# Kernel tuning notes

Hardware: AMD Instinct MI355X
Metric: run time of the kernel (lower is better)

## Reference

```python
import jax, jax.numpy as jnp
import numpy as np

B, N, C_IN = 4, 48, 32
HID = [32, 32]          # hidden_channel_list
NB = [32, 32]           # neighborhood_channels
C_OUT = 16
N_BASIS = 6             # equivariant 2->2 basis ops used by SnConv2


def _masked(t, mask):
    # zero out entries for padded nodes; mask: B,n,n,n bool, t: B,n,n,n,C
    return jnp.where(mask[..., None], t, jnp.zeros((), t.dtype))


def snconv2(t, W, b):
    """Sn-equivariant 2nd-order conv on dims (1,2); dim 3 rides along.
    t: B,i,j,m,C.  W: [6, C_in, C_out], one mixing matrix per basis op."""
    n = t.shape[1]
    tT = jnp.swapaxes(t, 1, 2)                       # transpose op
    diag = jnp.einsum('biimc->bimc', t)              # diagonal, B,i,m,C
    rows = t.sum(axis=2) / n                         # row sums,  B,i,m,C
    cols = t.sum(axis=1) / n                         # col sums,  B,j,m,C
    tot = t.sum(axis=(1, 2)) / (n * n)               # total sum, B,m,C
    # contract small features BEFORE broadcasting back to 2nd order
    out = (jnp.einsum('bijmc,cd->bijmd', t, W[0])
           + jnp.einsum('bijmc,cd->bijmd', tT, W[1])
           + jnp.einsum('bimc,cd->bimd', diag, W[2])[:, :, None]
           + jnp.einsum('bimc,cd->bimd', rows, W[3])[:, :, None]
           + jnp.einsum('bjmc,cd->bjmd', cols, W[4])[:, None]
           + jnp.einsum('bmc,cd->bmd', tot, W[5])[:, None, None]
           + b)
    return out


def localconv2(t, Wv, bv, Ww, bw, Wo, bo):
    """LocalConv2, product_type='elementwise': per-channel message passing
    along the node dims: z[b,i,j] = sum_k v[b,i,k] * w[b,k,j] / n."""
    n = t.shape[1]
    v = jnp.einsum('bijmc,cd->bijmd', t, Wv) + bv
    w = jnp.einsum('bijmc,cd->bijmd', t, Ww) + bw
    z = jnp.einsum('bikmc,bkjmc->bijmc', v, w) / n
    return jnp.einsum('bijmc,cd->bijmd', z, Wo) + bo


def setup_inputs() -> dict:
    key = jax.random.key(0)
    ks = jax.random.split(key, 24)
    x = jax.random.normal(ks[0], (B, N, C_IN), dtype=jnp.float32)
    # graphs of unequal size: per-graph node counts in [N//2, N]
    sizes = jax.random.randint(ks[1], (B,), N // 2, N + 1)
    node_valid = jnp.arange(N)[None, :] < sizes[:, None]            # B,n
    mask = (node_valid[:, :, None, None]
            & node_valid[:, None, :, None]
            & node_valid[:, None, None, :])                          # B,n,n,n
    s = 0.05
    inp = {'x': x, 'mask': mask}
    cin = C_IN
    for li, (nch, cout) in enumerate(zip(NB, HID)):
        inp[f'basic_W{li}'] = s * jax.random.normal(ks[2 + 8 * li], (N_BASIS, cin, cin), dtype=jnp.float32)
        inp[f'basic_b{li}'] = jnp.zeros((cin,), jnp.float32)
        inp[f'lv_W{li}'] = s * jax.random.normal(ks[3 + 8 * li], (cin, nch), dtype=jnp.float32)
        inp[f'lv_b{li}'] = jnp.zeros((nch,), jnp.float32)
        inp[f'lw_W{li}'] = s * jax.random.normal(ks[4 + 8 * li], (cin, nch), dtype=jnp.float32)
        inp[f'lw_b{li}'] = jnp.zeros((nch,), jnp.float32)
        inp[f'lo_W{li}'] = s * jax.random.normal(ks[5 + 8 * li], (nch, cout), dtype=jnp.float32)
        inp[f'lo_b{li}'] = jnp.zeros((cout,), jnp.float32)
        cin = cout
    inp['final_W'] = s * jax.random.normal(ks[20], (N_BASIS, cin, C_OUT), dtype=jnp.float32)
    inp['final_b'] = jnp.zeros((C_OUT,), jnp.float32)
    return inp


def reference(x, mask,
              basic_W0, basic_b0, lv_W0, lv_b0, lw_W0, lw_b0, lo_W0, lo_b0,
              basic_W1, basic_b1, lv_W1, lv_b1, lw_W1, lw_b1, lo_W1, lo_b1,
              final_W, final_b):
    # order-3 outer product T[b,i,j,k,c] = x[b,i,c]*x[b,j,c]*x[b,k,c]
    t = (x[:, :, None, None, :] * x[:, None, :, None, :]) * x[:, None, None, :, :]
    t = _masked(t, mask)
    layers = [(basic_W0, basic_b0, lv_W0, lv_b0, lw_W0, lw_b0, lo_W0, lo_b0),
              (basic_W1, basic_b1, lv_W1, lv_b1, lw_W1, lw_b1, lo_W1, lo_b1)]
    for bw_, bb_, vw, vb, ww, wb, ow, ob in layers:
        t = _masked(snconv2(t, bw_, bb_), mask)
        t = localconv2(t, vw, vb, ww, wb, ow, ob)
        t = jax.nn.relu(t)
        t = _masked(t, mask)
    out = _masked(snconv2(t, final_W, final_b), mask)
    return out
```

## Files before the change

### kernel.cpp

```cpp
#include <hip/hip_runtime.h>
#include <cstdint>


namespace {

constexpr int nB = 4, nN = 48, nC = 32;
constexpr int SJ_ = nN * nC;
constexpr int SI_ = nN * SJ_;
constexpr long SB_ = (long)nN * SI_;
constexpr int RP_ = 294912;
constexpr int CP_ = 294912;
constexpr int TP_ = 6144;

__device__ __forceinline__ void decodePos(int p, int& b, int& i, int& j, int& m) {
    m = p % nN; int r = p / nN;
    j = r % nN; r /= nN;
    i = r % nN; b = r / nN;
}

__global__ __launch_bounds__(256) void k_prepcomp(
    const float* __restrict__ x, const void* __restrict__ maskp,
    float* __restrict__ vm, float* __restrict__ S,
    const float* __restrict__ Wb0, const float* __restrict__ bb0,
    const float* __restrict__ Wv0, const float* __restrict__ Ww0,
    const float* __restrict__ Wb1, const float* __restrict__ bb1,
    const float* __restrict__ Wv1, const float* __restrict__ Ww1,
    float* __restrict__ cW, float* __restrict__ cb, float* __restrict__ cWs)
{
    __shared__ float Ws[1024];
    __shared__ float vmL[nB * nN];
    const int tid = threadIdx.x;

    if (blockIdx.x == 4) {
        const unsigned int w0 = *(const unsigned int*)maskp;
        const bool is_byte = (w0 == 0x01010101u);
        if (tid < nB * nN) {
            int b = tid / nN, i = tid % nN;
            long idx = ((long)(b * nN + i) * nN + i) * nN + i;
            int bit;
            if (is_byte) bit = (((const unsigned char*)maskp)[idx] != 0);
            else         bit = (((const int*)maskp)[idx] != 0);
            float f = bit ? 1.f : 0.f;
            vm[tid] = f; vmL[tid] = f;
        }
        __syncthreads();
        if (tid < nB * nC) {
            int b = tid >> 5, c = tid & 31;
            float s = 0.f;
            for (int j = 0; j < nN; ++j) s += x[(b * nN + j) * nC + c] * vmL[b * nN + j];
            S[tid] = s;
        }
        return;
    }

    const int blk = blockIdx.x;
    const float* Wb = (blk < 2) ? Wb0 : Wb1;
    const float* bb = (blk < 2) ? bb0 : bb1;
    const float* Wr = (blk == 0) ? Wv0 : (blk == 1) ? Ww0 : (blk == 2) ? Wv1 : Ww1;
    for (int q = tid; q < 1024; q += 256) Ws[q] = Wr[q];
    __syncthreads();
    for (int q = tid; q < 6144; q += 256) {
        const int d = q & 31;
        const float* row = Wb + (q >> 5) * 32;
        float s = 0.f;
        #pragma unroll
        for (int e = 0; e < 32; ++e) s = fmaf(row[e], Ws[e * 32 + d], s);
        cW[blk * 6144 + q] = s;
    }
    if (blk < 2) {
        for (int q = tid; q < 1024; q += 256) {
            const int d = q & 31; const int c = q >> 5;
            const float* r0 = Wb + c * 32;
            const float* r1 = Wb + 1024 + c * 32;
            float s = 0.f;
            #pragma unroll
            for (int e = 0; e < 32; ++e) s = fmaf(r0[e] + r1[e], Ws[e * 32 + d], s);
            cWs[blk * 1024 + q] = s;
        }
    }
    if (tid < 32) {
        float s = 0.f;
        #pragma unroll
        for (int e = 0; e < 32; ++e) s = fmaf(bb[e], Ws[e * 32 + tid], s);
        cb[blk * 32 + tid] = s;
    }
}

__global__ __launch_bounds__(256) void k_mix0(
    const float* __restrict__ x, const float* __restrict__ S,
    const float* __restrict__ Wb_a, const float* __restrict__ bias_a,
    float* __restrict__ dr_a, float* __restrict__ cc_a, float* __restrict__ tb_a,
    const float* __restrict__ Wb_b, const float* __restrict__ bias_b,
    float* __restrict__ dr_b, float* __restrict__ cc_b, float* __restrict__ tb_b)
{
    const int set = (blockIdx.x >= 36);
    const float* Wb   = set ? Wb_b   : Wb_a;
// ... 63 lines not shown
    float* ccp = set ? cc_b : cc_a;
    float* tbp = set ? tb_b : tb_a;
    __shared__ float W2s[32 * DOUT], W3s[32 * DOUT], W4s[32 * DOUT], W5s[32 * DOUT], bs[DOUT];
    const int tid = threadIdx.x;
    for (int q = tid; q < 32 * DOUT; q += 256) {
        W2s[q] = Wb[2 * 32 * DOUT + q]; W3s[q] = Wb[3 * 32 * DOUT + q];
        W4s[q] = Wb[4 * 32 * DOUT + q]; W5s[q] = Wb[5 * 32 * DOUT + q];
    }
    if (tid < DOUT) bs[tid] = bias[tid];
    __syncthreads();
    const int id = (blockIdx.x - (set ? 36 : 0)) * 256 + tid;
    const int m = id % nN; int r = id / nN; const int i = r % nN; const int b = r / nN;
    float odr[DOUT], occ[DOUT];
    #pragma unroll
    for (int d = 0; d < DOUT; ++d) { odr[d] = 0.f; occ[d] = 0.f; }
    for (int c2 = 0; c2 < 32; ++c2) {
        size_t q = (size_t)id * 32 + c2;
        float dg = dgp[q];
        float rw = (rw2[q] + rw2[q + RP_]) * (1.f / nN);
        float cl = (cl2[q] + cl2[q + CP_]) * (1.f / nN);
        #pragma unroll
        for (int d = 0; d < DOUT; ++d) {
            odr[d] = fmaf(dg, W2s[c2 * DOUT + d], fmaf(rw, W3s[c2 * DOUT + d], odr[d]));
            occ[d] = fmaf(cl, W4s[c2 * DOUT + d], occ[d]);
        }
    }
    #pragma unroll
    for (int d = 0; d < DOUT; d += 4) {
        *(float4*)(drp + (size_t)id * DOUT + d) = make_float4(odr[d], odr[d+1], odr[d+2], odr[d+3]);
        *(float4*)(ccp + (size_t)id * DOUT + d) = make_float4(occ[d], occ[d+1], occ[d+2], occ[d+3]);
    }
    if (i == 0) {
        float ot[DOUT];
        #pragma unroll
        for (int d = 0; d < DOUT; ++d) ot[d] = bs[d];
        for (int c2 = 0; c2 < 32; ++c2) {
            size_t q = (size_t)(b * nN + m) * 32 + c2;
            float tv = (tt4[q] + tt4[q + TP_] + tt4[q + 2 * TP_] + tt4[q + 3 * TP_])
                       * (1.f / (nN * nN));
            #pragma unroll
            for (int d = 0; d < DOUT; ++d) ot[d] = fmaf(tv, W5s[c2 * DOUT + d], ot[d]);
        }
        for (int d = 0; d < DOUT; d += 4)
            *(float4*)(tbp + (size_t)(b * nN + m) * DOUT + d) = make_float4(ot[d], ot[d+1], ot[d+2], ot[d+3]);
    }
}

#define FMA4(ar, tv, w4)                       \
    ar[0] = fmaf(tv, w4.x, ar[0]);             \
    ar[1] = fmaf(tv, w4.y, ar[1]);             \
    ar[2] = fmaf(tv, w4.z, ar[2]);             \
    ar[3] = fmaf(tv, w4.w, ar[3]);

template <int MODE>
__global__ __launch_bounds__(256) void k_vw(
    const float* __restrict__ src, const float* __restrict__ vm,
    const float* __restrict__ drv, const float* __restrict__ ccv, const float* __restrict__ tbv,
    const float* __restrict__ drw, const float* __restrict__ ccw, const float* __restrict__ tbw,
    const float* __restrict__ Wv2, const float* __restrict__ Ww2,
    const float* __restrict__ bv, const float* __restrict__ bw,
    float* __restrict__ vout, float* __restrict__ wout)
{
    constexpr int CH = 64;
    constexpr int CS = CH * 34;
    constexpr int BUF = (MODE == 0) ? CS : 2 * CS;
    __shared__ float sT[2][BUF];
    __shared__ float wL[(MODE == 0) ? 2048 : 4096];
    const int tid = threadIdx.x;

    {
        float4* wl4 = (float4*)wL;
        for (int q = tid; q < 512; q += 256) wl4[q] = ((const float4*)Wv2)[q];
        if (MODE == 1)
            for (int q = tid; q < 512; q += 256) wl4[512 + q] = ((const float4*)Ww2)[q];
    }

    const int base0 = blockIdx.x * 9 * CH;
    float4 rA0, rA1, rB0, rB1;

    auto loadChunk = [&](int k) {
        const int cb = base0 + k * CH;
        {   const int q = tid; const int pl = q >> 3, cq = q & 7;
            const int p = cb + pl;
            if (MODE == 0) {
                int b, i, j, m; decodePos(p, b, i, j, m);
                float4 xi = *(const float4*)(src + (size_t)(b * nN + i) * nC + cq * 4);
                float4 xj = *(const float4*)(src + (size_t)(b * nN + j) * nC + cq * 4);
                float4 xm = *(const float4*)(src + (size_t)(b * nN + m) * nC + cq * 4);
                rA0.x = xi.x * xj.x * xm.x; rA0.y = xi.y * xj.y * xm.y;
                rA0.z = xi.z * xj.z * xm.z; rA0.w = xi.w * xj.w * xm.w;
            } else {
                rA0 = *(const float4*)(src + (size_t)p * nC + cq * 4);
                int b, i, j, m; decodePos(p, b, i, j, m);
                long pT = ((long)(b * nN + j) * nN + i) * nN + m;
                rB0 = *(const float4*)(src + pT * nC + cq * 4);
            }
        }
        {   const int q = 256 + tid; const int pl = q >> 3, cq = q & 7;
            const int p = cb + pl;
            if (MODE == 0) {
                int b, i, j, m; decodePos(p, b, i, j, m);
                float4 xi = *(const float4*)(src + (size_t)(b * nN + i) * nC + cq * 4);
                float4 xj = *(const float4*)(src + (size_t)(b * nN + j) * nC + cq * 4);
                float4 xm = *(const float4*)(src + (size_t)(b * nN + m) * nC + cq * 4);
                rA1.x = xi.x * xj.x * xm.x; rA1.y = xi.y * xj.y * xm.y;
                rA1.z = xi.z * xj.z * xm.z; rA1.w = xi.w * xj.w * xm.w;
            } else {
                rA1 = *(const float4*)(src + (size_t)p * nC + cq * 4);
                int b, i, j, m; decodePos(p, b, i, j, m);
                long pT = ((long)(b * nN + j) * nN + i) * nN + m;
                rB1 = *(const float4*)(src + pT * nC + cq * 4);
            }
        }
    };
    auto writeChunk = [&](int buf) {
        {   const int q = tid; const int o = (q >> 3) * 34 + (q & 7) * 4;
            sT[buf][o + 0] = rA0.x; sT[buf][o + 1] = rA0.y;
            sT[buf][o + 2] = rA0.z; sT[buf][o + 3] = rA0.w;
            if (MODE == 1) {
                sT[buf][CS + o + 0] = rB0.x; sT[buf][CS + o + 1] = rB0.y;
                sT[buf][CS + o + 2] = rB0.z; sT[buf][CS + o + 3] = rB0.w;
            }
        }
        {   const int q = 256 + tid; const int o = (q >> 3) * 34 + (q & 7) * 4;
            sT[buf][o + 0] = rA1.x; sT[buf][o + 1] = rA1.y;
            sT[buf][o + 2] = rA1.z; sT[buf][o + 3] = rA1.w;
            if (MODE == 1) {
                sT[buf][CS + o + 0] = rB1.x; sT[buf][CS + o + 1] = rB1.y;
                sT[buf][CS + o + 2] = rB1.z; sT[buf][CS + o + 3] = rB1.w;
            }
        }
    };

    loadChunk(0);
    writeChunk(0);
    __syncthreads();

    const int pt = tid >> 3, dq = tid & 7;
    const int p0 = pt * 2, d0 = dq * 4;

    for (int k = 0; k < 9; ++k) {
        const int cur = k & 1;
        if (k < 8) loadChunk(k + 1);
        __builtin_amdgcn_sched_barrier(0);

        float accv[2][4], accw[2][4];
        #pragma unroll
        for (int l = 0; l < 2; ++l)
            #pragma unroll
            for (int d = 0; d < 4; ++d) { accv[l][d] = 0.f; accw[l][d] = 0.f; }

        const float* sp = sT[cur];
        #pragma unroll
        for (int cp = 0; cp < 16; ++cp) {
            float2 t0 = *(const float2*)(sp + (p0 + 0) * 34 + cp * 2);
            float2 t1 = *(const float2*)(sp + (p0 + 1) * 34 + cp * 2);
            const int c0 = cp * 2, c1 = cp * 2 + 1;
            const float* wwb = (MODE == 0) ? (wL + 1024) : (wL + 2048);
            float4 wv0 = *(const float4*)(wL + c0 * nC + d0);
            float4 wv1 = *(const float4*)(wL + c1 * nC + d0);
            float4 ww0 = *(const float4*)(wwb + c0 * nC + d0);
            float4 ww1 = *(const float4*)(wwb + c1 * nC + d0);
            FMA4(accv[0], t0.x, wv0); FMA4(accv[1], t1.x, wv0);
            FMA4(accv[0], t0.y, wv1); FMA4(accv[1], t1.y, wv1);
            FMA4(accw[0], t0.x, ww0); FMA4(accw[1], t1.x, ww0);
            FMA4(accw[0], t0.y, ww1); FMA4(accw[1], t1.y, ww1);
        }
        if (MODE == 1) {
            #pragma unroll
            for (int cp = 0; cp < 16; ++cp) {
                float2 t0 = *(const float2*)(sp + CS + (p0 + 0) * 34 + cp * 2);
                float2 t1 = *(const float2*)(sp + CS + (p0 + 1) * 34 + cp * 2);
                const int c0 = cp * 2, c1 = cp * 2 + 1;
                float4 wv0 = *(const float4*)(wL + 1024 + c0 * nC + d0);
                float4 wv1 = *(const float4*)(wL + 1024 + c1 * nC + d0);
                float4 ww0 = *(const float4*)(wL + 3072 + c0 * nC + d0);
                float4 ww1 = *(const float4*)(wL + 3072 + c1 * nC + d0);
                FMA4(accv[0], t0.x, wv0); FMA4(accv[1], t1.x, wv0);
                FMA4(accv[0], t0.y, wv1); FMA4(accv[1], t1.y, wv1);
                FMA4(accw[0], t0.x, ww0); FMA4(accw[1], t1.x, ww0);
                FMA4(accw[0], t0.y, ww1); FMA4(accw[1], t1.y, ww1);
            }
        }

        const int cb = base0 + k * CH;
        {
            float4 b4 = *(const float4*)(bv + d0);
            #pragma unroll
            for (int l = 0; l < 2; ++l) {
                int p = cb + p0 + l;
                int b, i, j, m; decodePos(p, b, i, j, m);
                float4 d4 = *(const float4*)(drv + (size_t)((b * nN + i) * nN + m) * nC + d0);
                float4 c4 = *(const float4*)(ccv + (size_t)((b * nN + j) * nN + m) * nC + d0);
                float4 t4 = *(const float4*)(tbv + (size_t)(b * nN + m) * nC + d0);
                float mk = vm[b * nN + i] * vm[b * nN + j] * vm[b * nN + m];
                float4 o4;
                o4.x = (accv[l][0] + d4.x + c4.x + t4.x) * mk + b4.x;
                o4.y = (accv[l][1] + d4.y + c4.y + t4.y) * mk + b4.y;
                o4.z = (accv[l][2] + d4.z + c4.z + t4.z) * mk + b4.z;
                o4.w = (accv[l][3] + d4.w + c4.w + t4.w) * mk + b4.w;
                *(float4*)(vout + (size_t)p * nC + d0) = o4;
            }
        }
        {
            float4 b4 = *(const float4*)(bw + d0);
            #pragma unroll
            for (int l = 0; l < 2; ++l) {
                int p = cb + p0 + l;
                int b, i, j, m; decodePos(p, b, i, j, m);
                float4 d4 = *(const float4*)(drw + (size_t)((b * nN + i) * nN + m) * nC + d0);
                float4 c4 = *(const float4*)(ccw + (size_t)((b * nN + j) * nN + m) * nC + d0);
                float4 t4 = *(const float4*)(tbw + (size_t)(b * nN + m) * nC + d0);
                float mk = vm[b * nN + i] * vm[b * nN + j] * vm[b * nN + m];
                float4 o4;
                o4.x = (accw[l][0] + d4.x + c4.x + t4.x) * mk + b4.x;
                o4.y = (accw[l][1] + d4.y + c4.y + t4.y) * mk + b4.y;
                o4.z = (accw[l][2] + d4.z + c4.z + t4.z) * mk + b4.z;
                o4.w = (accw[l][3] + d4.w + c4.w + t4.w) * mk + b4.w;
                *(float4*)(wout + (size_t)p * nC + d0) = o4;
            }
        }

        if (k < 8) {
            writeChunk((k + 1) & 1);
            __syncthreads();
        }
    }
}

__global__ __launch_bounds__(256, 3) void k_z(
    const float* __restrict__ v, const float* __restrict__ w,
    const float* __restrict__ Wo, const float* __restrict__ bo,
    const float* __restrict__ vm, float* __restrict__ tout,
    float* __restrict__ rows2, float* __restrict__ cols2,
    float* __restrict__ diag_, float* __restrict__ tot4)
{
    __shared__ float lds[12912];
    constexpr int HB = 6456;
    constexpr int ZS = 34;
    constexpr int ZWO = 9792;
    constexpr int TOT0 = 10816;
    const int tid = threadIdx.x;
    const int idb = blockIdx.x;
    const int xcd = idb & 7; const int qq = idb >> 3;
    const int tl = qq & 3; const int bm = (qq >> 2) * 8 + xcd;
    const int it = tl >> 1, jt = tl & 1;
    const int b = bm / nN, m = bm % nN;
    const int c = tid & 31;
    const int g = tid >> 5;
    const int i3 = g >> 1, j2 = g & 1;
    const int il0 = i3 * 6, jl0 = j2 * 12;
    const size_t posbase = (size_t)b * SB_ + (size_t)m * nC;

    const int q0 = tid, q1 = 256 + tid, q2 = 512 + tid;
    const int pV0 = q0 >> 3, pV1 = q1 >> 3, pV2 = q2 >> 3;
    const int cq0 = (q0 & 7) * 4, cq1 = (q1 & 7) * 4, cq2 = (q2 & 7) * 4;
    const int iiV0 = pV0 >> 2, kkV0 = pV0 & 3;
    const int iiV1 = pV1 >> 2, kkV1 = pV1 & 3;
    const int iiV2 = pV2 >> 2, kkV2 = pV2 & 3;
    const int kkW0 = pV0 / 24, jjW0 = pV0 - kkW0 * 24;
    const int kkW1 = pV1 / 24, jjW1 = pV1 - kkW1 * 24;
    const int kkW2 = pV2 / 24, jjW2 = pV2 - kkW2 * 24;
    const float* vs0 = v + posbase + (size_t)(it * 24 + iiV0) * SI_ + (size_t)kkV0 * SJ_ + cq0;
    const float* vs1 = v + posbase + (size_t)(it * 24 + iiV1) * SI_ + (size_t)kkV1 * SJ_ + cq1;
    const float* vs2 = v + posbase + (size_t)(it * 24 + iiV2) * SI_ + (size_t)kkV2 * SJ_ + cq2;
    const float* ws0 = w + posbase + (size_t)kkW0 * SI_ + (size_t)(jt * 24 + jjW0) * SJ_ + cq0;
    const float* ws1 = w + posbase + (size_t)kkW1 * SI_ + (size_t)(jt * 24 + jjW1) * SJ_ + cq1;
    const float* ws2 = w + posbase + (size_t)kkW2 * SI_ + (size_t)(jt * 24 + jjW2) * SJ_ + cq2;
    const int dV0 = kkV0 * 807 + cq0 * 25 + iiV0;
    const int dV1 = kkV1 * 807 + cq1 * 25 + iiV1;
    const int dV2 = kkV2 * 807 + cq2 * 25 + iiV2;
    const int dW0 = 3228 + kkW0 * 807 + cq0 * 25 + jjW0;
    const int dW1 = 3228 + kkW1 * 807 + cq1 * 25 + jjW1;
    const int dW2 = 3228 + kkW2 * 807 + cq2 * 25 + jjW2;

    float4 rv0, rv1, rv2, rw0, rw1, rw2;

    auto loadChunk = [&](int ch) {
// ... 103 lines not shown
            float4 o4;
            o4.x = fmaxf(oac[u][0] + b4.x, 0.f) * mk;
            o4.y = fmaxf(oac[u][1] + b4.y, 0.f) * mk;
            o4.z = fmaxf(oac[u][2] + b4.z, 0.f) * mk;
            o4.w = fmaxf(oac[u][3] + b4.w, 0.f) * mk;
            *(float4*)(tout + posbase + (size_t)gi * SI_ + (size_t)gj * SJ_ + d0) = o4;
            *(float2*)(lds + p * ZS + d0) = make_float2(o4.x, o4.y);
            *(float2*)(lds + p * ZS + d0 + 2) = make_float2(o4.z, o4.w);
        }
        __syncthreads();

        for (int rd = 0; rd < 2; ++rd) {
            int task = rd * 256 + tid;
            if (task < 384) {
                int i_r = task >> 5, c_r = task & 31;
                float rsum = 0.f;
                #pragma unroll
                for (int jl = 0; jl < 24; ++jl) rsum += lds[(i_r * 24 + jl) * ZS + c_r];
                int gi = it * 24 + 12 * h + i_r;
                rows2[(size_t)jt * RP_ + ((size_t)(b * nN + gi) * nN + m) * nC + c_r] = rsum;
                totacc += rsum;
                if (it == jt)
                    diag_[((size_t)(b * nN + gi) * nN + m) * nC + c_r] =
                        lds[(i_r * 24 + (12 * h + i_r)) * ZS + c_r];
            }
        }
        #pragma unroll
        for (int rr = 0; rr < 3; ++rr) {
            int task = rr * 256 + tid;
            int jl = task >> 5, c_c = task & 31;
            float csum = 0.f;
            #pragma unroll
            for (int il = 0; il < 12; ++il) csum += lds[(il * 24 + jl) * ZS + c_c];
            colacc[rr] += csum;
        }
    }

    #pragma unroll
    for (int rr = 0; rr < 3; ++rr) {
        int task = rr * 256 + tid;
        int jl = task >> 5, c_c = task & 31;
        cols2[(size_t)it * CP_ + ((size_t)(b * nN + jt * 24 + jl) * nN + m) * nC + c_c] = colacc[rr];
    }
    lds[TOT0 + g * 32 + c] = totacc;
    __syncthreads();
    if (tid < 32) {
        float s = 0.f;
        #pragma unroll
        for (int gg = 0; gg < 8; ++gg) s += lds[TOT0 + gg * 32 + tid];
        tot4[(size_t)(it * 2 + jt) * TP_ + (size_t)(b * nN + m) * nC + tid] = s;
    }
}

__global__ __launch_bounds__(256) void k_final(
    const float* __restrict__ t, const float* __restrict__ vm,
    const float* __restrict__ drp, const float* __restrict__ ccp, const float* __restrict__ tbp,
    const float* __restrict__ W0, const float* __restrict__ W1,
    float* __restrict__ out)
{
    constexpr int CH = 64, CS = CH * 34;
    __shared__ float sT[2][2 * CS];
    __shared__ float wL[1024];
    const int tid = threadIdx.x;

    {
        float4* wl4 = (float4*)wL;
        for (int q = tid; q < 128; q += 256) wl4[q] = ((const float4*)W0)[q];
        for (int q = tid; q < 128; q += 256) wl4[128 + q] = ((const float4*)W1)[q];
    }

    const int base0 = blockIdx.x * 9 * CH;
    float4 rA0, rA1, rB0, rB1;

    auto loadChunk = [&](int k) {
        const int cb = base0 + k * CH;
        {   const int q = tid; const int pl = q >> 3, cq = q & 7;
            const int p = cb + pl;
            rA0 = *(const float4*)(t + (size_t)p * nC + cq * 4);
            int b, i, j, m; decodePos(p, b, i, j, m);
            long pT = ((long)(b * nN + j) * nN + i) * nN + m;
            rB0 = *(const float4*)(t + pT * nC + cq * 4);
        }
        {   const int q = 256 + tid; const int pl = q >> 3, cq = q & 7;
            const int p = cb + pl;
            rA1 = *(const float4*)(t + (size_t)p * nC + cq * 4);
            int b, i, j, m; decodePos(p, b, i, j, m);
            long pT = ((long)(b * nN + j) * nN + i) * nN + m;
            rB1 = *(const float4*)(t + pT * nC + cq * 4);
        }
    };
    auto writeChunk = [&](int buf) {
        {   const int q = tid; const int o = (q >> 3) * 34 + (q & 7) * 4;
            sT[buf][o + 0] = rA0.x; sT[buf][o + 1] = rA0.y;
            sT[buf][o + 2] = rA0.z; sT[buf][o + 3] = rA0.w;
            sT[buf][CS + o + 0] = rB0.x; sT[buf][CS + o + 1] = rB0.y;
            sT[buf][CS + o + 2] = rB0.z; sT[buf][CS + o + 3] = rB0.w;
        }
        {   const int q = 256 + tid; const int o = (q >> 3) * 34 + (q & 7) * 4;
            sT[buf][o + 0] = rA1.x; sT[buf][o + 1] = rA1.y;
            sT[buf][o + 2] = rA1.z; sT[buf][o + 3] = rA1.w;
            sT[buf][CS + o + 0] = rB1.x; sT[buf][CS + o + 1] = rB1.y;
            sT[buf][CS + o + 2] = rB1.z; sT[buf][CS + o + 3] = rB1.w;
        }
    };

    loadChunk(0);
    writeChunk(0);
    __syncthreads();

    const int pt = tid >> 3, dq = tid & 7;
    const int p0 = pt * 2, d0 = dq * 2;

    for (int k = 0; k < 9; ++k) {
        const int cur = k & 1;
        if (k < 8) loadChunk(k + 1);
        __builtin_amdgcn_sched_barrier(0);

        float acc[2][2];
        acc[0][0] = 0.f; acc[0][1] = 0.f; acc[1][0] = 0.f; acc[1][1] = 0.f;
        const float* sp = sT[cur];
        #pragma unroll
        for (int cp = 0; cp < 16; ++cp) {
            float2 t0 = *(const float2*)(sp + (p0 + 0) * 34 + cp * 2);
            float2 t1 = *(const float2*)(sp + (p0 + 1) * 34 + cp * 2);
            const int c0 = cp * 2, c1 = cp * 2 + 1;
            float2 w0 = *(const float2*)(wL + c0 * 16 + d0);
            float2 w1 = *(const float2*)(wL + c1 * 16 + d0);
            acc[0][0] = fmaf(t0.x, w0.x, acc[0][0]); acc[0][1] = fmaf(t0.x, w0.y, acc[0][1]);
            acc[1][0] = fmaf(t1.x, w0.x, acc[1][0]); acc[1][1] = fmaf(t1.x, w0.y, acc[1][1]);
            acc[0][0] = fmaf(t0.y, w1.x, acc[0][0]); acc[0][1] = fmaf(t0.y, w1.y, acc[0][1]);
            acc[1][0] = fmaf(t1.y, w1.x, acc[1][0]); acc[1][1] = fmaf(t1.y, w1.y, acc[1][1]);
        }
        #pragma unroll
        for (int cp = 0; cp < 16; ++cp) {
            float2 t0 = *(const float2*)(sp + CS + (p0 + 0) * 34 + cp * 2);
            float2 t1 = *(const float2*)(sp + CS + (p0 + 1) * 34 + cp * 2);
            const int c0 = cp * 2, c1 = cp * 2 + 1;
            float2 w0 = *(const float2*)(wL + 512 + c0 * 16 + d0);
            float2 w1 = *(const float2*)(wL + 512 + c1 * 16 + d0);
            acc[0][0] = fmaf(t0.x, w0.x, acc[0][0]); acc[0][1] = fmaf(t0.x, w0.y, acc[0][1]);
            acc[1][0] = fmaf(t1.x, w0.x, acc[1][0]); acc[1][1] = fmaf(t1.x, w0.y, acc[1][1]);
            acc[0][0] = fmaf(t0.y, w1.x, acc[0][0]); acc[0][1] = fmaf(t0.y, w1.y, acc[0][1]);
            acc[1][0] = fmaf(t1.y, w1.x, acc[1][0]); acc[1][1] = fmaf(t1.y, w1.y, acc[1][1]);
        }

        const int cb = base0 + k * CH;
        #pragma unroll
        for (int l = 0; l < 2; ++l) {
            int p = cb + p0 + l;
            int b, i, j, m; decodePos(p, b, i, j, m);
            float2 d2 = *(const float2*)(drp + (size_t)((b * nN + i) * nN + m) * 16 + d0);
            float2 cc2 = *(const float2*)(ccp + (size_t)((b * nN + j) * nN + m) * 16 + d0);
            float2 tb2 = *(const float2*)(tbp + (size_t)(b * nN + m) * 16 + d0);
            float mk = vm[b * nN + i] * vm[b * nN + j] * vm[b * nN + m];
            float2 o2;
            o2.x = (acc[l][0] + d2.x + cc2.x + tb2.x) * mk;
            o2.y = (acc[l][1] + d2.y + cc2.y + tb2.y) * mk;
            *(float2*)(out + (size_t)p * 16 + d0) = o2;
        }

        if (k < 8) {
            writeChunk((k + 1) & 1);
            __syncthreads();
        }
    }
}

}

extern "C" void kernel_launch(void* const* d_in, const int* in_sizes, int n_in,
                              void* d_out, int out_size, void* d_ws, size_t ws_size,
                              hipStream_t stream)
{
    (void)in_sizes; (void)n_in; (void)out_size; (void)ws_size;
    const float* x    = (const float*)d_in[0];
    const void*  mask = d_in[1];
    const float* bW0  = (const float*)d_in[2];
    const float* bb0  = (const float*)d_in[3];
    const float* lvW0 = (const float*)d_in[4];
    const float* lvb0 = (const float*)d_in[5];
    const float* lwW0 = (const float*)d_in[6];
    const float* lwb0 = (const float*)d_in[7];
    const float* loW0 = (const float*)d_in[8];
    const float* lob0 = (const float*)d_in[9];
    const float* bW1  = (const float*)d_in[10];
    const float* bb1  = (const float*)d_in[11];
    const float* lvW1 = (const float*)d_in[12];
    const float* lvb1 = (const float*)d_in[13];
    const float* lwW1 = (const float*)d_in[14];
    const float* lwb1 = (const float*)d_in[15];
    const float* loW1 = (const float*)d_in[16];
    const float* lob1 = (const float*)d_in[17];
    const float* fW   = (const float*)d_in[18];
    const float* fb   = (const float*)d_in[19];

    float* ws  = (float*)d_ws;
    float* t     = ws;
    float* v     = ws + 14155776L;
    float* w     = ws + 28311552L;
    float* rows2 = ws + 42467328L;
    float* cols2 = rows2 + 2 * 294912;
    float* diag  = cols2 + 2 * 294912;
    float* tot4  = diag + 294912;
    float* drv   = tot4 + 4 * 6144;
    float* ccv   = drv + 294912;
    float* tbv   = ccv + 294912;
    float* drw   = tbv + 6144;
    float* ccw   = drw + 294912;
    float* tbw   = ccw + 294912;
    float* cW    = tbw + 6144;
    float* cb    = cW + 4 * 6144;
    float* cWs   = cb + 128;
    float* S     = cWs + 2048;
    float* vm    = S + 128;
    float* out   = (float*)d_out;

    k_prepcomp<<<5, 256, 0, stream>>>(x, mask, vm, S,
                                      bW0, bb0, lvW0, lwW0,
                                      bW1, bb1, lvW1, lwW1, cW, cb, cWs);

    k_mix0<<<72, 256, 0, stream>>>(x, S,
                                   cW + 0,    cb + 0,  drv, ccv, tbv,
                                   cW + 6144, cb + 32, drw, ccw, tbw);
    k_vw<0><<<768, 256, 0, stream>>>(x, vm, drv, ccv, tbv, drw, ccw, tbw,
                                     cWs,
                                     cWs,
                                     lvb0, lwb0, v, w);
    k_z<<<768, 256, 0, stream>>>(v, w, loW0, lob0, vm, t, rows2, cols2, diag, tot4);

    k_mix<32><<<72, 256, 0, stream>>>(diag, rows2, cols2, tot4,
                                      cW + 12288, cb + 64, drv, ccv, tbv,
                                      cW + 18432, cb + 96, drw, ccw, tbw);
    k_vw<1><<<768, 256, 0, stream>>>(t, vm, drv, ccv, tbv, drw, ccw, tbw,
                                     cW + 12288,
                                     cW + 18432,
                                     lvb1, lwb1, v, w);
    k_z<<<768, 256, 0, stream>>>(v, w, loW1, lob1, vm, t, rows2, cols2, diag, tot4);

    k_mix<16><<<36, 256, 0, stream>>>(diag, rows2, cols2, tot4,
                                      fW, fb, drv, ccv, tbv,
                                      fW, fb, drv, ccv, tbv);
    k_final<<<768, 256, 0, stream>>>(t, vm, drv, ccv, tbv, fW, fW + 512, out);
}
```

Measured before the change: 462.4 us.

## Process (i,j)/(j,i) row pairs together to share transposed loads in snconv

The layer-1 v/w kernel and the final snconv kernel now assign each work chunk a pair of mirrored rows (i,j) and (j,i), or two diagonal rows, taken from a precomputed pair table. Both rows are loaded into shared memory once, so the transpose term reads the partner row from LDS and no separate transposed gather is needed. This roughly halves global reads of the 2nd-order tensor in these kernels. In exchange it adds descriptor decoding, a pair-table build in the prep kernel, and a different block count for the final kernel.

```diff
diff --git a/kernel.cpp b/kernel.cpp
--- a/kernel.cpp
+++ b/kernel.cpp
@@ -18,9 +18,25 @@
     i = r % nN; b = r / nN;
 }
 
+#define MAKE_DESC(cgx, _bA,_iA,_jA,_bB,_iB,_jB,_md,_baseA,_baseB) do {        \
+    if ((cgx) < 4512) {                                                        \
+        int pr_ = (cgx) >> 2; int bb_ = (cgx) & 3;                             \
+        int ij_ = pairTab[pr_];                                                \
+        _iA = ij_ & 255; _jA = ij_ >> 8; _bA = bb_;                            \
+        _iB = _jA; _jB = _iA; _bB = bb_; _md = 48;                             \
+    } else {                                                                   \
+        int dg_ = (cgx) - 4512;                                                \
+        int u0_ = 2 * dg_, u1_ = u0_ + 1;                                      \
+        _bA = u0_ / 48; _iA = u0_ - _bA * 48; _jA = _iA;                       \
+        _bB = u1_ / 48; _iB = u1_ - _bB * 48; _jB = _iB; _md = 0;              \
+    }                                                                          \
+    _baseA = (_bA * 48 + _iA) * 48 + _jA;                                      \
+    _baseB = (_bB * 48 + _iB) * 48 + _jB;                                      \
+} while (0)
+
 __global__ __launch_bounds__(256) void k_prepcomp(
     const float* __restrict__ x, const void* __restrict__ maskp,
-    float* __restrict__ vm, float* __restrict__ S,
+    float* __restrict__ vm, float* __restrict__ S, int* __restrict__ pairTab,
     const float* __restrict__ Wb0, const float* __restrict__ bb0,
     const float* __restrict__ Wv0, const float* __restrict__ Ww0,
     const float* __restrict__ Wb1, const float* __restrict__ bb1,
@@ -42,6 +58,12 @@
             else         bit = (((const int*)maskp)[idx] != 0);
             float f = bit ? 1.f : 0.f;
             vm[tid] = f; vmL[tid] = f;
+        }
+        for (int k = tid; k < 1128; k += 256) {
+            int i = 0, a2 = 0;
+            while (a2 + (47 - i) <= k) { a2 += 47 - i; ++i; }
+            int j = i + 1 + (k - a2);
+            pairTab[k] = i | (j << 8);
         }
         __syncthreads();
         if (tid < nB * nC) {
@@ -211,83 +233,57 @@
     ar[2] = fmaf(tv, w4.z, ar[2]);             \
     ar[3] = fmaf(tv, w4.w, ar[3]);
 
-template <int MODE>
-__global__ __launch_bounds__(256) void k_vw(
+__global__ __launch_bounds__(256) void k_vw0(
     const float* __restrict__ src, const float* __restrict__ vm,
     const float* __restrict__ drv, const float* __restrict__ ccv, const float* __restrict__ tbv,
     const float* __restrict__ drw, const float* __restrict__ ccw, const float* __restrict__ tbw,
-    const float* __restrict__ Wv2, const float* __restrict__ Ww2,
+    const float* __restrict__ Wv2,
     const float* __restrict__ bv, const float* __restrict__ bw,
     float* __restrict__ vout, float* __restrict__ wout)
 {
     constexpr int CH = 64;
     constexpr int CS = CH * 34;
-    constexpr int BUF = (MODE == 0) ? CS : 2 * CS;
-    __shared__ float sT[2][BUF];
-    __shared__ float wL[(MODE == 0) ? 2048 : 4096];
+    __shared__ float sT[2][CS];
+    __shared__ float wL[2048];
     const int tid = threadIdx.x;
 
     {
         float4* wl4 = (float4*)wL;
         for (int q = tid; q < 512; q += 256) wl4[q] = ((const float4*)Wv2)[q];
-        if (MODE == 1)
-            for (int q = tid; q < 512; q += 256) wl4[512 + q] = ((const float4*)Ww2)[q];
     }
 
     const int base0 = blockIdx.x * 9 * CH;
-    float4 rA0, rA1, rB0, rB1;
+    float4 rA0, rA1;
 
     auto loadChunk = [&](int k) {
         const int cb = base0 + k * CH;
         {   const int q = tid; const int pl = q >> 3, cq = q & 7;
             const int p = cb + pl;
-            if (MODE == 0) {
-                int b, i, j, m; decodePos(p, b, i, j, m);
-                float4 xi = *(const float4*)(src + (size_t)(b * nN + i) * nC + cq * 4);
-                float4 xj = *(const float4*)(src + (size_t)(b * nN + j) * nC + cq * 4);
-                float4 xm = *(const float4*)(src + (size_t)(b * nN + m) * nC + cq * 4);
-                rA0.x = xi.x * xj.x * xm.x; rA0.y = xi.y * xj.y * xm.y;
-                rA0.z = xi.z * xj.z * xm.z; rA0.w = xi.w * xj.w * xm.w;
-            } else {
-                rA0 = *(const float4*)(src + (size_t)p * nC + cq * 4);
-                int b, i, j, m; decodePos(p, b, i, j, m);
-                long pT = ((long)(b * nN + j) * nN + i) * nN + m;
-                rB0 = *(const float4*)(src + pT * nC + cq * 4);
-            }
+            int b, i, j, m; decodePos(p, b, i, j, m);
+            float4 xi = *(const float4*)(src + (size_t)(b * nN + i) * nC + cq * 4);
+            float4 xj = *(const float4*)(src + (size_t)(b * nN + j) * nC + cq * 4);
+            float4 xm = *(const float4*)(src + (size_t)(b * nN + m) * nC + cq * 4);
+            rA0.x = xi.x * xj.x * xm.x; rA0.y = xi.y * xj.y * xm.y;
+            rA0.z = xi.z * xj.z * xm.z; rA0.w = xi.w * xj.w * xm.w;
         }
         {   const int q = 256 + tid; const int pl = q >> 3, cq = q & 7;
             const int p = cb + pl;
-            if (MODE == 0) {
-                int b, i, j, m; decodePos(p, b, i, j, m);
-                float4 xi = *(const float4*)(src + (size_t)(b * nN + i) * nC + cq * 4);
-                float4 xj = *(const float4*)(src + (size_t)(b * nN + j) * nC + cq * 4);
-                float4 xm = *(const float4*)(src + (size_t)(b * nN + m) * nC + cq * 4);
-                rA1.x = xi.x * xj.x * xm.x; rA1.y = xi.y * xj.y * xm.y;
-                rA1.z = xi.z * xj.z * xm.z; rA1.w = xi.w * xj.w * xm.w;
-            } else {
-                rA1 = *(const float4*)(src + (size_t)p * nC + cq * 4);
-                int b, i, j, m; decodePos(p, b, i, j, m);
-                long pT = ((long)(b * nN + j) * nN + i) * nN + m;
-                rB1 = *(const float4*)(src + pT * nC + cq * 4);
-            }
+            int b, i, j, m; decodePos(p, b, i, j, m);
+            float4 xi = *(const float4*)(src + (size_t)(b * nN + i) * nC + cq * 4);
+            float4 xj = *(const float4*)(src + (size_t)(b * nN + j) * nC + cq * 4);
+            float4 xm = *(const float4*)(src + (size_t)(b * nN + m) * nC + cq * 4);
+            rA1.x = xi.x * xj.x * xm.x; rA1.y = xi.y * xj.y * xm.y;
+            rA1.z = xi.z * xj.z * xm.z; rA1.w = xi.w * xj.w * xm.w;
         }
     };
     auto writeChunk = [&](int buf) {
         {   const int q = tid; const int o = (q >> 3) * 34 + (q & 7) * 4;
             sT[buf][o + 0] = rA0.x; sT[buf][o + 1] = rA0.y;
             sT[buf][o + 2] = rA0.z; sT[buf][o + 3] = rA0.w;
-            if (MODE == 1) {
-                sT[buf][CS + o + 0] = rB0.x; sT[buf][CS + o + 1] = rB0.y;
-                sT[buf][CS + o + 2] = rB0.z; sT[buf][CS + o + 3] = rB0.w;
-            }
         }
         {   const int q = 256 + tid; const int o = (q >> 3) * 34 + (q & 7) * 4;
             sT[buf][o + 0] = rA1.x; sT[buf][o + 1] = rA1.y;
             sT[buf][o + 2] = rA1.z; sT[buf][o + 3] = rA1.w;
-            if (MODE == 1) {
-                sT[buf][CS + o + 0] = rB1.x; sT[buf][CS + o + 1] = rB1.y;
-                sT[buf][CS + o + 2] = rB1.z; sT[buf][CS + o + 3] = rB1.w;
-            }
         }
     };
 
@@ -315,31 +311,14 @@
             float2 t0 = *(const float2*)(sp + (p0 + 0) * 34 + cp * 2);
             float2 t1 = *(const float2*)(sp + (p0 + 1) * 34 + cp * 2);
             const int c0 = cp * 2, c1 = cp * 2 + 1;
-            const float* wwb = (MODE == 0) ? (wL + 1024) : (wL + 2048);
             float4 wv0 = *(const float4*)(wL + c0 * nC + d0);
             float4 wv1 = *(const float4*)(wL + c1 * nC + d0);
-            float4 ww0 = *(const float4*)(wwb + c0 * nC + d0);
-            float4 ww1 = *(const float4*)(wwb + c1 * nC + d0);
+            float4 ww0 = *(const float4*)(wL + 1024 + c0 * nC + d0);
+            float4 ww1 = *(const float4*)(wL + 1024 + c1 * nC + d0);
             FMA4(accv[0], t0.x, wv0); FMA4(accv[1], t1.x, wv0);
             FMA4(accv[0], t0.y, wv1); FMA4(accv[1], t1.y, wv1);
             FMA4(accw[0], t0.x, ww0); FMA4(accw[1], t1.x, ww0);
             FMA4(accw[0], t0.y, ww1); FMA4(accw[1], t1.y, ww1);
-        }
-        if (MODE == 1) {
-            #pragma unroll
-            for (int cp = 0; cp < 16; ++cp) {
-                float2 t0 = *(const float2*)(sp + CS + (p0 + 0) * 34 + cp * 2);
-                float2 t1 = *(const float2*)(sp + CS + (p0 + 1) * 34 + cp * 2);
-                const int c0 = cp * 2, c1 = cp * 2 + 1;
-                float4 wv0 = *(const float4*)(wL + 1024 + c0 * nC + d0);
-                float4 wv1 = *(const float4*)(wL + 1024 + c1 * nC + d0);
-                float4 ww0 = *(const float4*)(wL + 3072 + c0 * nC + d0);
-                float4 ww1 = *(const float4*)(wL + 3072 + c1 * nC + d0);
-                FMA4(accv[0], t0.x, wv0); FMA4(accv[1], t1.x, wv0);
-                FMA4(accv[0], t0.y, wv1); FMA4(accv[1], t1.y, wv1);
-                FMA4(accw[0], t0.x, ww0); FMA4(accw[1], t1.x, ww0);
-                FMA4(accw[0], t0.y, ww1); FMA4(accw[1], t1.y, ww1);
-            }
         }
 
         const int cb = base0 + k * CH;
@@ -383,6 +362,145 @@
         if (k < 8) {
             writeChunk((k + 1) & 1);
             __syncthreads();
+        }
+    }
+}
+
+__global__ __launch_bounds__(256) void k_vwp(
+    const float* __restrict__ src, const float* __restrict__ vm,
+    const int* __restrict__ pairTab,
+    const float* __restrict__ drv, const float* __restrict__ ccv, const float* __restrict__ tbv,
+    const float* __restrict__ drw, const float* __restrict__ ccw, const float* __restrict__ tbw,
+    const float* __restrict__ Wv2, const float* __restrict__ Ww2,
+    const float* __restrict__ bv, const float* __restrict__ bw,
+    float* __restrict__ vout, float* __restrict__ wout)
+{
+    __shared__ float sT[2][96 * 34];
+    __shared__ float wL[4096];
+    const int tid = threadIdx.x;
+
+    {
+        float4* wl4 = (float4*)wL;
+        for (int q = tid; q < 512; q += 256) wl4[q] = ((const float4*)Wv2)[q];
+        for (int q = tid; q < 512; q += 256) wl4[512 + q] = ((const float4*)Ww2)[q];
+    }
+
+    const int cg0 = blockIdx.x * 6;
+    float4 rq0, rq1, rq2;
+
+    auto loadQ = [&](int qi, int baseA, int baseB) -> float4 {
+        const int g = (qi >= 384);
+        const int base = g ? baseB : baseA;
+        const int off = (qi - (g ? 384 : 0)) * 4;
+        return *(const float4*)(src + (size_t)base * 1536 + off);
+    };
+    auto writeQ = [&](float* buf, int qi, float4 r) {
+        const int g = (qi >= 384);
+        const int row = g * 48 + ((qi - g * 384) >> 3);
+        const int o = row * 34 + (qi & 7) * 4;
+        buf[o + 0] = r.x; buf[o + 1] = r.y; buf[o + 2] = r.z; buf[o + 3] = r.w;
+    };
+
+    int bA, iA, jA, bB, iB, jB, md, baseA, baseB;
+    MAKE_DESC(cg0, bA, iA, jA, bB, iB, jB, md, baseA, baseB);
+    rq0 = loadQ(tid, baseA, baseB);
+    rq1 = loadQ(tid + 256, baseA, baseB);
+    rq2 = loadQ(tid + 512, baseA, baseB);
+    writeQ(sT[0], tid, rq0); writeQ(sT[0], tid + 256, rq1); writeQ(sT[0], tid + 512, rq2);
+    __syncthreads();
+
+    const int pt = tid >> 3, dq = tid & 7;
+    const int p0 = pt * 3, d0 = dq * 4;
+    const float4 bv4 = *(const float4*)(bv + d0);
+    const float4 bw4 = *(const float4*)(bw + d0);
+
+    for (int c = 0; c < 6; ++c) {
+        int nbA = 0, niA = 0, njA = 0, nbB = 0, niB = 0, njB = 0, nmd = 0, nbaseA = 0, nbaseB = 0;
+        if (c < 5) {
+            MAKE_DESC(cg0 + c + 1, nbA, niA, njA, nbB, niB, njB, nmd, nbaseA, nbaseB);
+            rq0 = loadQ(tid, nbaseA, nbaseB);
+            rq1 = loadQ(tid + 256, nbaseA, nbaseB);
+            rq2 = loadQ(tid + 512, nbaseA, nbaseB);
+        }
+        __builtin_amdgcn_sched_barrier(0);
+
+        float accv[3][4], accw[3][4];
+        #pragma unroll
+        for (int l = 0; l < 3; ++l)
+            #pragma unroll
+            for (int d = 0; d < 4; ++d) { accv[l][d] = 0.f; accw[l][d] = 0.f; }
+
+        const float* sp = sT[c & 1];
+        const int mir0 = (pt < 16) ? (p0 + md) : (p0 - md);
+        #pragma unroll
+        for (int cp = 0; cp < 16; ++cp) {
+            const int c0 = cp * 2, c1 = c0 + 1;
+            float2 a0 = *(const float2*)(sp + (p0 + 0) * 34 + c0);
+            float2 a1 = *(const float2*)(sp + (p0 + 1) * 34 + c0);
+            float2 a2 = *(const float2*)(sp + (p0 + 2) * 34 + c0);
+            float2 e0 = *(const float2*)(sp + (mir0 + 0) * 34 + c0);
+            float2 e1 = *(const float2*)(sp + (mir0 + 1) * 34 + c0);
+            float2 e2 = *(const float2*)(sp + (mir0 + 2) * 34 + c0);
+            float4 wav0 = *(const float4*)(wL + c0 * nC + d0);
+            float4 wav1 = *(const float4*)(wL + c1 * nC + d0);
+            float4 wbv0 = *(const float4*)(wL + 1024 + c0 * nC + d0);
+            float4 wbv1 = *(const float4*)(wL + 1024 + c1 * nC + d0);
+            float4 waw0 = *(const float4*)(wL + 2048 + c0 * nC + d0);
+            float4 waw1 = *(const float4*)(wL + 2048 + c1 * nC + d0);
+            float4 wbw0 = *(const float4*)(wL + 3072 + c0 * nC + d0);
+            float4 wbw1 = *(const float4*)(wL + 3072 + c1 * nC + d0);
+            FMA4(accv[0], a0.x, wav0); FMA4(accv[0], a0.y, wav1);
+            FMA4(accv[1], a1.x, wav0); FMA4(accv[1], a1.y, wav1);
+            FMA4(accv[2], a2.x, wav0); FMA4(accv[2], a2.y, wav1);
+            FMA4(accv[0], e0.x, wbv0); FMA4(accv[0], e0.y, wbv1);
+            FMA4(accv[1], e1.x, wbv0); FMA4(accv[1], e1.y, wbv1);
+            FMA4(accv[2], e2.x, wbv0); FMA4(accv[2], e2.y, wbv1);
+            FMA4(accw[0], a0.x, waw0); FMA4(accw[0], a0.y, waw1);
+            FMA4(accw[1], a1.x, waw0); FMA4(accw[1], a1.y, waw1);
+            FMA4(accw[2], a2.x, waw0); FMA4(accw[2], a2.y, waw1);
+            FMA4(accw[0], e0.x, wbw0); FMA4(accw[0], e0.y, wbw1);
+            FMA4(accw[1], e1.x, wbw0); FMA4(accw[1], e1.y, wbw1);
+            FMA4(accw[2], e2.x, wbw0); FMA4(accw[2], e2.y, wbw1);
+        }
+
+        const int gb = (pt < 16) ? bA : bB;
+        const int gi = (pt < 16) ? iA : iB;
+        const int gj = (pt < 16) ? jA : jB;
+        const int gbase = (pt < 16) ? baseA : baseB;
+        const int m0 = p0 - ((pt < 16) ? 0 : 48);
+        const float vmi = vm[gb * nN + gi];
+        const float vmj = vm[gb * nN + gj];
+        #pragma unroll
+        for (int l = 0; l < 3; ++l) {
+            const int m = m0 + l;
+            const float mk = vmi * vmj * vm[gb * nN + m];
+            float4 d4 = *(const float4*)(drv + (size_t)((gb * nN + gi) * nN + m) * nC + d0);
+            float4 c4 = *(const float4*)(ccv + (size_t)((gb * nN + gj) * nN + m) * nC + d0);
+            float4 t4 = *(const float4*)(tbv + (size_t)(gb * nN + m) * nC + d0);
+            const size_t po = ((size_t)gbase * 48 + m) * nC + d0;
+            float4 o4;
+            o4.x = (accv[l][0] + d4.x + c4.x + t4.x) * mk + bv4.x;
+            o4.y = (accv[l][1] + d4.y + c4.y + t4.y) * mk + bv4.y;
+            o4.z = (accv[l][2] + d4.z + c4.z + t4.z) * mk + bv4.z;
+            o4.w = (accv[l][3] + d4.w + c4.w + t4.w) * mk + bv4.w;
+            *(float4*)(vout + po) = o4;
+            float4 d4w = *(const float4*)(drw + (size_t)((gb * nN + gi) * nN + m) * nC + d0);
+            float4 c4w = *(const float4*)(ccw + (size_t)((gb * nN + gj) * nN + m) * nC + d0);
+            float4 t4w = *(const float4*)(tbw + (size_t)(gb * nN + m) * nC + d0);
+            float4 o4w;
+            o4w.x = (accw[l][0] + d4w.x + c4w.x + t4w.x) * mk + bw4.x;
+            o4w.y = (accw[l][1] + d4w.y + c4w.y + t4w.y) * mk + bw4.y;
+            o4w.z = (accw[l][2] + d4w.z + c4w.z + t4w.z) * mk + bw4.z;
+            o4w.w = (accw[l][3] + d4w.w + c4w.w + t4w.w) * mk + bw4.w;
+            *(float4*)(wout + po) = o4w;
+        }
+
+        if (c < 5) {
+            float* nb = sT[(c + 1) & 1];
+            writeQ(nb, tid, rq0); writeQ(nb, tid + 256, rq1); writeQ(nb, tid + 512, rq2);
+            __syncthreads();
+            bA = nbA; iA = niA; jA = njA; bB = nbB; iB = niB; jB = njB;
+            md = nmd; baseA = nbaseA; baseB = nbaseB;
         }
     }
 }
@@ -592,14 +710,14 @@
     }
 }
 
-__global__ __launch_bounds__(256) void k_final(
-    const float* __restrict__ t, const float* __restrict__ vm,
+__global__ __launch_bounds__(256) void k_finalp(
+    const float* __restrict__ src, const float* __restrict__ vm,
+    const int* __restrict__ pairTab,
     const float* __restrict__ drp, const float* __restrict__ ccp, const float* __restrict__ tbp,
     const float* __restrict__ W0, const float* __restrict__ W1,
     float* __restrict__ out)
 {
-    constexpr int CH = 64, CS = CH * 34;
-    __shared__ float sT[2][2 * CS];
+    __shared__ float sT[2][96 * 34];
     __shared__ float wL[1024];
     const int tid = threadIdx.x;
 
@@ -609,99 +727,96 @@
         for (int q = tid; q < 128; q += 256) wl4[128 + q] = ((const float4*)W1)[q];
     }
 
-    const int base0 = blockIdx.x * 9 * CH;
-    float4 rA0, rA1, rB0, rB1;
-
-    auto loadChunk = [&](int k) {
-        const int cb = base0 + k * CH;
-        {   const int q = tid; const int pl = q >> 3, cq = q & 7;
-            const int p = cb + pl;
-            rA0 = *(const float4*)(t + (size_t)p * nC + cq * 4);
-            int b, i, j, m; decodePos(p, b, i, j, m);
-            long pT = ((long)(b * nN + j) * nN + i) * nN + m;
-            rB0 = *(const float4*)(t + pT * nC + cq * 4);
-        }
-        {   const int q = 256 + tid; const int pl = q >> 3, cq = q & 7;
-            const int p = cb + pl;
-            rA1 = *(const float4*)(t + (size_t)p * nC + cq * 4);
-            int b, i, j, m; decodePos(p, b, i, j, m);
-            long pT = ((long)(b * nN + j) * nN + i) * nN + m;
-            rB1 = *(const float4*)(t + pT * nC + cq * 4);
-        }
+    const int cg0 = blockIdx.x * 4;
+    float4 rq0, rq1, rq2;
+
+    auto loadQ = [&](int qi, int baseA, int baseB) -> float4 {
+        const int g = (qi >= 384);
+        const int base = g ? baseB : baseA;
+        const int off = (qi - (g ? 384 : 0)) * 4;
+        return *(const float4*)(src + (size_t)base * 1536 + off);
     };
-    auto writeChunk = [&](int buf) {
-        {   const int q = tid; const int o = (q >> 3) * 34 + (q & 7) * 4;
-            sT[buf][o + 0] = rA0.x; sT[buf][o + 1] = rA0.y;
-            sT[buf][o + 2] = rA0.z; sT[buf][o + 3] = rA0.w;
-            sT[buf][CS + o + 0] = rB0.x; sT[buf][CS + o + 1] = rB0.y;
-            sT[buf][CS + o + 2] = rB0.z; sT[buf][CS + o + 3] = rB0.w;
-        }
-        {   const int q = 256 + tid; const int o = (q >> 3) * 34 + (q & 7) * 4;
-            sT[buf][o + 0] = rA1.x; sT[buf][o + 1] = rA1.y;
-            sT[buf][o + 2] = rA1.z; sT[buf][o + 3] = rA1.w;
-            sT[buf][CS + o + 0] = rB1.x; sT[buf][CS + o + 1] = rB1.y;
-            sT[buf][CS + o + 2] = rB1.z; sT[buf][CS + o + 3] = rB1.w;
-        }
+    auto writeQ = [&](float* buf, int qi, float4 r) {
+        const int g = (qi >= 384);
+        const int row = g * 48 + ((qi - g * 384) >> 3);
+        const int o = row * 34 + (qi & 7) * 4;
+        buf[o + 0] = r.x; buf[o + 1] = r.y; buf[o + 2] = r.z; buf[o + 3] = r.w;
     };
 
-    loadChunk(0);
-    writeChunk(0);
+    int bA, iA, jA, bB, iB, jB, md, baseA, baseB;
+    MAKE_DESC(cg0, bA, iA, jA, bB, iB, jB, md, baseA, baseB);
+    rq0 = loadQ(tid, baseA, baseB);
+    rq1 = loadQ(tid + 256, baseA, baseB);
+    rq2 = loadQ(tid + 512, baseA, baseB);
+    writeQ(sT[0], tid, rq0); writeQ(sT[0], tid + 256, rq1); writeQ(sT[0], tid + 512, rq2);
     __syncthreads();
 
     const int pt = tid >> 3, dq = tid & 7;
-    const int p0 = pt * 2, d0 = dq * 2;
-
-    for (int k = 0; k < 9; ++k) {
-        const int cur = k & 1;
-        if (k < 8) loadChunk(k + 1);
+    const int p0 = pt * 3, d0 = dq * 2;
+
+    for (int c = 0; c < 4; ++c) {
+        int nbA = 0, niA = 0, njA = 0, nbB = 0, niB = 0, njB = 0, nmd = 0, nbaseA = 0, nbaseB = 0;
+        if (c < 3) {
+            MAKE_DESC(cg0 + c + 1, nbA, niA, njA, nbB, niB, njB, nmd, nbaseA, nbaseB);
+            rq0 = loadQ(tid, nbaseA, nbaseB);
+            rq1 = loadQ(tid + 256, nbaseA, nbaseB);
+            rq2 = loadQ(tid + 512, nbaseA, nbaseB);
+        }
         __builtin_amdgcn_sched_barrier(0);
 
-        float acc[2][2];
-        acc[0][0] = 0.f; acc[0][1] = 0.f; acc[1][0] = 0.f; acc[1][1] = 0.f;
-        const float* sp = sT[cur];
+        float acc[3][2];
+        #pragma unroll
+        for (int l = 0; l < 3; ++l) { acc[l][0] = 0.f; acc[l][1] = 0.f; }
+
+        const float* sp = sT[c & 1];
+        const int mir0 = (pt < 16) ? (p0 + md) : (p0 - md);
         #pragma unroll
         for (int cp = 0; cp < 16; ++cp) {
-            float2 t0 = *(const float2*)(sp + (p0 + 0) * 34 + cp * 2);
-            float2 t1 = *(const float2*)(sp + (p0 + 1) * 34 + cp * 2);
-            const int c0 = cp * 2, c1 = cp * 2 + 1;
-            float2 w0 = *(const float2*)(wL + c0 * 16 + d0);
-            float2 w1 = *(const float2*)(wL + c1 * 16 + d0);
-            acc[0][0] = fmaf(t0.x, w0.x, acc[0][0]); acc[0][1] = fmaf(t0.x, w0.y, acc[0][1]);
-            acc[1][0] = fmaf(t1.x, w0.x, acc[1][0]); acc[1][1] = fmaf(t1.x, w0.y, acc[1][1]);
-            acc[0][0] = fmaf(t0.y, w1.x, acc[0][0]); acc[0][1] = fmaf(t0.y, w1.y, acc[0][1]);
-            acc[1][0] = fmaf(t1.y, w1.x, acc[1][0]); acc[1][1] = fmaf(t1.y, w1.y, acc[1][1]);
-        }
-        #pragma unroll
-        for (int cp = 0; cp < 16; ++cp) {
-            float2 t0 = *(const float2*)(sp + CS + (p0 + 0) * 34 + cp * 2);
-            float2 t1 = *(const float2*)(sp + CS + (p0 + 1) * 34 + cp * 2);
-            const int c0 = cp * 2, c1 = cp * 2 + 1;
-            float2 w0 = *(const float2*)(wL + 512 + c0 * 16 + d0);
-            float2 w1 = *(const float2*)(wL + 512 + c1 * 16 + d0);
-            acc[0][0] = fmaf(t0.x, w0.x, acc[0][0]); acc[0][1] = fmaf(t0.x, w0.y, acc[0][1]);
-            acc[1][0] = fmaf(t1.x, w0.x, acc[1][0]); acc[1][1] = fmaf(t1.x, w0.y, acc[1][1]);
-            acc[0][0] = fmaf(t0.y, w1.x, acc[0][0]); acc[0][1] = fmaf(t0.y, w1.y, acc[0][1]);
-            acc[1][0] = fmaf(t1.y, w1.x, acc[1][0]); acc[1][1] = fmaf(t1.y, w1.y, acc[1][1]);
-        }
-
-        const int cb = base0 + k * CH;
-        #pragma unroll
-        for (int l = 0; l < 2; ++l) {
-            int p = cb + p0 + l;
-            int b, i, j, m; decodePos(p, b, i, j, m);
-            float2 d2 = *(const float2*)(drp + (size_t)((b * nN + i) * nN + m) * 16 + d0);
-            float2 cc2 = *(const float2*)(ccp + (size_t)((b * nN + j) * nN + m) * 16 + d0);
-            float2 tb2 = *(const float2*)(tbp + (size_t)(b * nN + m) * 16 + d0);
-            float mk = vm[b * nN + i] * vm[b * nN + j] * vm[b * nN + m];
+            const int c0 = cp * 2, c1 = c0 + 1;
+            float2 a0 = *(const float2*)(sp + (p0 + 0) * 34 + c0);
+            float2 a1 = *(const float2*)(sp + (p0 + 1) * 34 + c0);
+            float2 a2 = *(const float2*)(sp + (p0 + 2) * 34 + c0);
+            float2 e0 = *(const float2*)(sp + (mir0 + 0) * 34 + c0);
+            float2 e1 = *(const float2*)(sp + (mir0 + 1) * 34 + c0);
+            float2 e2 = *(const float2*)(sp + (mir0 + 2) * 34 + c0);
+            float2 w00 = *(const float2*)(wL + c0 * 16 + d0);
+            float2 w01 = *(const float2*)(wL + c1 * 16 + d0);
+            float2 w10 = *(const float2*)(wL + 512 + c0 * 16 + d0);
+            float2 w11 = *(const float2*)(wL + 512 + c1 * 16 + d0);
+            acc[0][0] = fmaf(a0.x, w00.x, fmaf(a0.y, w01.x, fmaf(e0.x, w10.x, fmaf(e0.y, w11.x, acc[0][0]))));
+            acc[0][1] = fmaf(a0.x, w00.y, fmaf(a0.y, w01.y, fmaf(e0.x, w10.y, fmaf(e0.y, w11.y, acc[0][1]))));
+            acc[1][0] = fmaf(a1.x, w00.x, fmaf(a1.y, w01.x, fmaf(e1.x, w10.x, fmaf(e1.y, w11.x, acc[1][0]))));
+            acc[1][1] = fmaf(a1.x, w00.y, fmaf(a1.y, w01.y, fmaf(e1.x, w10.y, fmaf(e1.y, w11.y, acc[1][1]))));
+            acc[2][0] = fmaf(a2.x, w00.x, fmaf(a2.y, w01.x, fmaf(e2.x, w10.x, fmaf(e2.y, w11.x, acc[2][0]))));
+            acc[2][1] = fmaf(a2.x, w00.y, fmaf(a2.y, w01.y, fmaf(e2.x, w10.y, fmaf(e2.y, w11.y, acc[2][1]))));
+        }
+
+        const int gb = (pt < 16) ? bA : bB;
+        const int gi = (pt < 16) ? iA : iB;
+        const int gj = (pt < 16) ? jA : jB;
+        const int gbase = (pt < 16) ? baseA : baseB;
+        const int m0 = p0 - ((pt < 16) ? 0 : 48);
+        const float vmi = vm[gb * nN + gi];
+        const float vmj = vm[gb * nN + gj];
+        #pragma unroll
+        for (int l = 0; l < 3; ++l) {
+            const int m = m0 + l;
+            const float mk = vmi * vmj * vm[gb * nN + m];
+            float2 d2 = *(const float2*)(drp + (size_t)((gb * nN + gi) * nN + m) * 16 + d0);
+            float2 c2 = *(const float2*)(ccp + (size_t)((gb * nN + gj) * nN + m) * 16 + d0);
+            float2 t2 = *(const float2*)(tbp + (size_t)(gb * nN + m) * 16 + d0);
             float2 o2;
-            o2.x = (acc[l][0] + d2.x + cc2.x + tb2.x) * mk;
-            o2.y = (acc[l][1] + d2.y + cc2.y + tb2.y) * mk;
-            *(float2*)(out + (size_t)p * 16 + d0) = o2;
-        }
-
-        if (k < 8) {
-            writeChunk((k + 1) & 1);
+            o2.x = (acc[l][0] + d2.x + c2.x + t2.x) * mk;
+            o2.y = (acc[l][1] + d2.y + c2.y + t2.y) * mk;
+            *(float2*)(out + ((size_t)gbase * 48 + m) * 16 + d0) = o2;
+        }
+
+        if (c < 3) {
+            float* nb = sT[(c + 1) & 1];
+            writeQ(nb, tid, rq0); writeQ(nb, tid + 256, rq1); writeQ(nb, tid + 512, rq2);
             __syncthreads();
+            bA = nbA; iA = niA; jA = njA; bB = nbB; iB = niB; jB = njB;
+            md = nmd; baseA = nbaseA; baseB = nbaseB;
         }
     }
 }
@@ -753,32 +868,33 @@
     float* cWs   = cb + 128;
     float* S     = cWs + 2048;
     float* vm    = S + 128;
+    int*   pairTab = (int*)(vm + 192);
     float* out   = (float*)d_out;
 
-    k_prepcomp<<<5, 256, 0, stream>>>(x, mask, vm, S,
+    k_prepcomp<<<5, 256, 0, stream>>>(x, mask, vm, S, pairTab,
                                       bW0, bb0, lvW0, lwW0,
                                       bW1, bb1, lvW1, lwW1, cW, cb, cWs);
 
     k_mix0<<<72, 256, 0, stream>>>(x, S,
                                    cW + 0,    cb + 0,  drv, ccv, tbv,
                                    cW + 6144, cb + 32, drw, ccw, tbw);
-    k_vw<0><<<768, 256, 0, stream>>>(x, vm, drv, ccv, tbv, drw, ccw, tbw,
-                                     cWs,
-                                     cWs,
-                                     lvb0, lwb0, v, w);
+    k_vw0<<<768, 256, 0, stream>>>(x, vm, drv, ccv, tbv, drw, ccw, tbw,
+                                   cWs,
+                                   lvb0, lwb0, v, w);
     k_z<<<768, 256, 0, stream>>>(v, w, loW0, lob0, vm, t, rows2, cols2, diag, tot4);
 
     k_mix<32><<<72, 256, 0, stream>>>(diag, rows2, cols2, tot4,
                                       cW + 12288, cb + 64, drv, ccv, tbv,
                                       cW + 18432, cb + 96, drw, ccw, tbw);
-    k_vw<1><<<768, 256, 0, stream>>>(t, vm, drv, ccv, tbv, drw, ccw, tbw,
-                                     cW + 12288,
-                                     cW + 18432,
-                                     lvb1, lwb1, v, w);
+    k_vwp<<<768, 256, 0, stream>>>(t, vm, pairTab, drv, ccv, tbv, drw, ccw, tbw,
+                                   cW + 12288,
+                                   cW + 18432,
+                                   lvb1, lwb1, v, w);
     k_z<<<768, 256, 0, stream>>>(v, w, loW1, lob1, vm, t, rows2, cols2, diag, tot4);
 
     k_mix<16><<<36, 256, 0, stream>>>(diag, rows2, cols2, tot4,
                                       fW, fb, drv, ccv, tbv,
                                       fW, fb, drv, ccv, tbv);
-    k_final<<<768, 256, 0, stream>>>(t, vm, drv, ccv, tbv, fW, fW + 512, out);
+    k_finalp<<<1152, 256, 0, stream>>>(t, vm, pairTab, drv, ccv, tbv,
+                                       fW, fW + 512, out);
 }
```

New measurement: 468.1 us, median of 2. Within noise of the previous version (+1.2%).
